# Kernel optimization log

Hardware: AMD Instinct MI355X
Metric: run time of the kernel (lower is better)

Reference implementation:

```python
import jax, jax.numpy as jnp
import numpy as np

K = 8
NUM_BLOCKS = 4
ALPHA = K / (K + 1)  # 8/9


def _knn_norm_adj(xyz, k):
    """xyz: (B, 3, N) -> symmetric-normalized GCN adjacency (B, N, N).

    Mirrors knn_point(k, xyz, xyz) -> indices[:, 1:] -> get_adjacency_matrix,
    then the (input-independent) DenseGCNConv normalization: self loops set to 1,
    deg clamped >= 1, D^-1/2 A D^-1/2. adj is identical for every GCN call, so
    it is normalized once here.
    """
    x2 = jnp.sum(xyz * xyz, axis=1)                       # (B, N)
    inner = jnp.einsum('bci,bcj->bij', xyz, xyz)          # (B, N, N)
    dist = x2[:, :, None] + x2[:, None, :] - 2.0 * inner  # squared pairwise dist
    _, idx = jax.lax.top_k(-dist, k)                      # (B, N, k); self (dist 0) first
    nbr = idx[:, :, 1:]                                   # drop self -> k-1 neighbors
    B, N = x2.shape
    adj = jnp.zeros((B, N, N), xyz.dtype)
    adj = adj.at[jnp.arange(B)[:, None, None],
                 jnp.arange(N)[None, :, None], nbr].set(1.0)
    ar = jnp.arange(N)
    adj = adj.at[:, ar, ar].set(1.0)                      # add_loop=True
    dis = jnp.clip(jnp.sum(adj, axis=-1), 1.0, None) ** -0.5  # (B, N)
    return dis[:, :, None] * adj * dis[:, None, :]


def setup_inputs() -> dict:
    key = jax.random.key(0)
    ks = jax.random.split(key, 6)
    B, N, C = 16, 2048, 128
    s = 1.0 / np.sqrt(C).astype(np.float32)
    return {
        'xyz': jax.random.normal(ks[0], (B, 3, N), jnp.float32),
        'points': jax.random.normal(ks[1], (B, C, N), jnp.float32),
        'Wc': jax.random.normal(ks[2], (4, C, C), jnp.float32) * s,   # nn.Linear weights (out,in)
        'Wg': jax.random.normal(ks[3], (4, C, C), jnp.float32) * s,   # DenseGCNConv lin weights
        'Wuc': jax.random.normal(ks[4], (6, C), jnp.float32) * s,
        'Wug': jax.random.normal(ks[5], (6, C), jnp.float32) * s,
    }


def reference(xyz, points, Wc, Wg, Wuc, Wug):
    adj = _knn_norm_adj(xyz, K)                 # (B, N, N)
    pts = jnp.swapaxes(points, 1, 2)            # (B, N, C) channel-last internally
    for i in range(NUM_BLOCKS):
        shortcut = pts
        act = jax.nn.relu(pts)
        center = jnp.einsum('bnc,dc->bnd', act, Wc[i])                 # Linear on relu(points)
        grouped = adj @ jnp.einsum('bnc,dc->bnd', shortcut, Wg[i])     # DenseGCNConv on shortcut
        pts = (1.0 - ALPHA) * grouped + ALPHA * center + shortcut
    # unpool head
    points_xyz = jnp.einsum('bnd,od->bno', pts, Wuc)                   # (B, N, 6)
    grouped_xyz = adj @ jnp.einsum('bnd,od->bno', pts, Wug)            # (B, N, 6)
    new = ALPHA * points_xyz + (1.0 - ALPHA) * grouped_xyz
    B, N, _ = new.shape
    new = jnp.swapaxes(new, 1, 2).reshape(B, 3, 2, N) + xyz[:, :, None, :]
    new_xyz = new.reshape(B, 3, 2 * N)
    return new_xyz, jnp.swapaxes(pts, 1, 2)     # ((B,3,2N), (B,C,N))
```

## Files before the change

### kernel.cpp

```cpp
#include <hip/hip_runtime.h>
#include <hip/hip_bf16.h>

static constexpr int NB = 16;
static constexpr int NP = 2048;
static constexpr int NC = 128;
#define ALPHA_F ((float)(8.0/9.0))
#define OMA_F   ((float)(1.0 - 8.0/9.0))

typedef __attribute__((ext_vector_type(8))) short bfrag;
typedef __attribute__((ext_vector_type(4))) float ffrag;

union BU { bfrag v; uint4 u; unsigned int w[4]; };

__device__ inline void split2(float x, float y, unsigned& hi, unsigned& lo) {
    __hip_bfloat162 h = __float22bfloat162_rn(make_float2(x, y));
    float2 hb = __bfloat1622float2(h);
    __hip_bfloat162 l = __float22bfloat162_rn(make_float2(x - hb.x, y - hb.y));
    __builtin_memcpy(&hi, &h, 4);
    __builtin_memcpy(&lo, &l, 4);
}

__device__ inline void split1(float x, unsigned short& h, unsigned short& l) {
    __hip_bfloat16 hb = __float2bfloat16(x);
    float hf = __bfloat162float(hb);
    __hip_bfloat16 lb = __float2bfloat16(x - hf);
    __builtin_memcpy(&h, &hb, 2);
    __builtin_memcpy(&l, &lb, 2);
}

__global__ __launch_bounds__(256) void knn_kernel(const float* __restrict__ xyz,
                                                  int* __restrict__ nbr) {
    __shared__ float4 sp[NP];
    __shared__ float  md[64][33];
    __shared__ int    mi[64][33];
    int b = blockIdx.y;
    const float* X = xyz + (size_t)b * 3 * NP;
    for (int m = threadIdx.x; m < NP; m += 256) {
        float x = X[m], y = X[NP + m], z = X[2 * NP + m];
        sp[m] = make_float4(x, y, z, x * x + y * y + z * z);
    }
    __syncthreads();

    int tid = threadIdx.x;
    int p = tid >> 2;
    int q = tid & 3;
    int base = blockIdx.x * 64;
    int n = base + p;
    float4 me = sp[n];
    float xi = me.x, yi = me.y, zi = me.z, qi = me.w;

    float gd[8]; int gi[8];
#pragma unroll
    for (int t = 0; t < 8; ++t) { gd[t] = 3.4e38f; gi[t] = 0; }
#pragma unroll 1
    for (int g = 0; g < 64; ++g) {
        float gm = 3.4e38f;
#pragma unroll
        for (int i = 0; i < 8; ++i) {
            int j = (g * 8 + i) * 4 + q;
            float4 c4v = sp[j];
            float inner = xi * c4v.x + yi * c4v.y + zi * c4v.z;
            float d = qi + c4v.w - 2.0f * inner;
            gm = fminf(gm, d);
        }
        bool c[8];
#pragma unroll
        for (int t = 0; t < 8; ++t) c[t] = gm < gd[t];
#pragma unroll
        for (int t = 7; t >= 1; --t) {
            gd[t] = c[t - 1] ? gd[t - 1] : (c[t] ? gm : gd[t]);
            gi[t] = c[t - 1] ? gi[t - 1] : (c[t] ? g : gi[t]);
        }
        gd[0] = c[0] ? gm : gd[0];
        gi[0] = c[0] ? g : gi[0];
    }

    unsigned long long mask = 0ull;
#pragma unroll
    for (int t = 0; t < 8; ++t) mask |= (1ull << gi[t]);

    float bd[8]; int bi[8];
#pragma unroll
    for (int t = 0; t < 8; ++t) { bd[t] = 3.4e38f; bi[t] = 0; }
    while (mask) {
        int g = (int)__builtin_ctzll(mask);
        mask &= (mask - 1ull);
#pragma unroll
        for (int i = 0; i < 8; ++i) {
            int j = (g * 8 + i) * 4 + q;
            float4 c4v = sp[j];
            float inner = xi * c4v.x + yi * c4v.y + zi * c4v.z;
            float d = qi + c4v.w - 2.0f * inner;
            bool c[8];
#pragma unroll
            for (int t = 0; t < 8; ++t) c[t] = d < bd[t];
#pragma unroll
            for (int t = 7; t >= 1; --t) {
                bd[t] = c[t - 1] ? bd[t - 1] : (c[t] ? d : bd[t]);
                bi[t] = c[t - 1] ? bi[t - 1] : (c[t] ? j : bi[t]);
            }
            bd[0] = c[0] ? d : bd[0];
            bi[0] = c[0] ? j : bi[0];
        }
    }
#pragma unroll
    for (int t = 0; t < 8; ++t) {
        md[p][q * 8 + t] = bd[t];
        mi[p][q * 8 + t] = bi[t];
    }
    __syncthreads();

    if (tid < 64) {
        float fd[8]; int fi[8];
#pragma unroll
        for (int t = 0; t < 8; ++t) { fd[t] = 3.4e38f; fi[t] = 0; }
#pragma unroll 4
        for (int cc = 0; cc < 32; ++cc) {
            float d = md[tid][cc];
            int j = mi[tid][cc];
            bool c[8];
#pragma unroll
            for (int t = 0; t < 8; ++t) c[t] = d < fd[t];
#pragma unroll
            for (int t = 7; t >= 1; --t) {
                fd[t] = c[t - 1] ? fd[t - 1] : (c[t] ? d : fd[t]);
                fi[t] = c[t - 1] ? fi[t - 1] : (c[t] ? j : fi[t]);
            }
            fd[0] = c[0] ? d : fd[0];
            fi[0] = c[0] ? j : fi[0];
        }
        int row = b * NP + base + tid;
#pragma unroll
        for (int t = 0; t < 7; ++t) nbr[row * 7 + t] = fi[t + 1];
    }
}

__global__ __launch_bounds__(256) void transpose_kernel(const float* __restrict__ in,
                                                        float* __restrict__ out,
                                                        int R, int S) {
    __shared__ float t[32][33];
    int b = blockIdx.z;
    int s0 = blockIdx.x * 32, r0 = blockIdx.y * 32;
    const float* I = in + (size_t)b * R * S;
    float* O = out + (size_t)b * R * S;
#pragma unroll
    for (int i = 0; i < 4; ++i) {
        int r = r0 + threadIdx.y + i * 8;
        t[threadIdx.y + i * 8][threadIdx.x] = I[(size_t)r * S + s0 + threadIdx.x];
    }
    __syncthreads();
#pragma unroll
    for (int i = 0; i < 4; ++i) {
        int s = s0 + threadIdx.y + i * 8;
        O[(size_t)s * R + r0 + threadIdx.x] = t[threadIdx.x][threadIdx.y + i * 8];
    }
}

__global__ __launch_bounds__(256) void prep_w_kernel(const float* __restrict__ Wc,
                                                     const float* __restrict__ Wg,
                                                     uint4* __restrict__ WP) {
    int t = blockIdx.x * 256 + threadIdx.x;
    int ncol = t & 127;
    int quad = (t >> 7) & 3;
    int s = (t >> 9) & 3;
    int mat = (t >> 11) & 1;
    int layer = t >> 12;
    const float* W = (mat ? Wg : Wc) + (size_t)layer * NC * NC + (size_t)ncol * NC + s * 32 + quad * 8;
    float4 a = *((const float4*)W);
    float4 b = *((const float4*)(W + 4));
    BU hi, lo;
    split2(a.x, a.y, hi.w[0], lo.w[0]);
    split2(a.z, a.w, hi.w[1], lo.w[1]);
    split2(b.x, b.y, hi.w[2], lo.w[2]);
    split2(b.z, b.w, hi.w[3], lo.w[3]);
    WP[t * 2] = hi.u;
    WP[t * 2 + 1] = lo.u;
}

template <int MODE>
__global__ __launch_bounds__(512) void gemm_fused_kernel(const float* __restrict__ Asrc,
                                                         const float* __restrict__ Y2in,
                                                         const int* __restrict__ nbr,
                                                         const uint4* __restrict__ WPc,
                                                         const uint4* __restrict__ WPg,
                                                         float* __restrict__ Zout,
                                                         float* __restrict__ Y2out) {
    __shared__ unsigned short AhT[64][136];
    __shared__ unsigned short AlT[64][136];
    __shared__ int s_nb[448];
    int tid = threadIdx.x;
    int wid = tid >> 6, lane = tid & 63;
    int quad = lane >> 4, l15 = lane & 15;
    int xcd = blockIdx.x & 7;
    int slot = blockIdx.x >> 3;
    int bb = xcd * 2 + (slot >> 5);
    int n0 = (slot & 31) << 6;
    size_t m0 = (size_t)bb * NP + n0;
    int ncol = wid * 16 + l15;

    BU Bch[4], Bcl[4], Bgh[4], Bgl[4];
#pragma unroll
    for (int s = 0; s < 4; ++s) {
        int idx = ((s * 4 + quad) * 128 + ncol) * 2;
        Bch[s].u = WPc[idx];
        Bcl[s].u = WPc[idx + 1];
        Bgh[s].u = WPg[idx];
        Bgl[s].u = WPg[idx + 1];
    }

    if (MODE == 1) {
        if (tid < 448) s_nb[tid] = nbr[m0 * 7 + tid];
        __syncthreads();
        size_t bbase = (size_t)bb * NP;
#pragma unroll 1
        for (int it = 0; it < 4; ++it) {
            int f = tid + it * 512;
            int r = f >> 5, c4 = (f & 31) * 4;
            size_t row = m0 + r;
            float4 z = *((const float4*)(Asrc + row * NC + c4));
            float4 acc = *((const float4*)(Y2in + row * NC + c4));
#pragma unroll
            for (int t = 0; t < 7; ++t) {
                int j = s_nb[r * 7 + t];
                float4 v = *((const float4*)(Y2in + (bbase + (size_t)j) * NC + c4));
                acc.x += v.x; acc.y += v.y; acc.z += v.z; acc.w += v.w;
            }
            float4 a;
            a.x = OMA_F * (0.125f * acc.x) + z.x;
            a.y = OMA_F * (0.125f * acc.y) + z.y;
            a.z = OMA_F * (0.125f * acc.z) + z.z;
            a.w = OMA_F * (0.125f * acc.w) + z.w;
            unsigned h01, l01, h23, l23;
            split2(a.x, a.y, h01, l01);
            split2(a.z, a.w, h23, l23);
            *((uint2*)&AhT[r][c4]) = make_uint2(h01, h23);
            *((uint2*)&AlT[r][c4]) = make_uint2(l01, l23);
        }
    } else {
#pragma unroll
        for (int it = 0; it < 4; ++it) {
            int f = tid + it * 512;
            int c = f >> 4, rq = (f & 15) * 4;
            float4 v = *((const float4*)(Asrc + ((size_t)bb * NC + c) * NP + n0 + rq));
            float vv[4] = {v.x, v.y, v.z, v.w};
#pragma unroll
            for (int k = 0; k < 4; ++k) {
                unsigned short h, l;
                split1(vv[k], h, l);
                AhT[rq + k][c] = h;
                AlT[rq + k][c] = l;
            }
        }
    }
    __syncthreads();

    ffrag accC[4], accG[4];
#pragma unroll
    for (int mt = 0; mt < 4; ++mt) { accC[mt] = (ffrag)0.0f; accG[mt] = (ffrag)0.0f; }

#pragma unroll
    for (int s = 0; s < 4; ++s) {
#pragma unroll
        for (int mt = 0; mt < 4; ++mt) {
            int m = mt * 16 + l15;
            int k = s * 32 + quad * 8;
            BU ah, al, rh, rl;
            ah.u = *((const uint4*)&AhT[m][k]);
            al.u = *((const uint4*)&AlT[m][k]);
#pragma unroll
            for (int w = 0; w < 4; ++w) {
                unsigned msk = ((ah.w[w] & 0x80008000u) >> 15) * 0xFFFFu;
                rh.w[w] = ah.w[w] & ~msk;
                rl.w[w] = al.w[w] & ~msk;
            }
            accC[mt] = __builtin_amdgcn_mfma_f32_16x16x32_bf16(rh.v, Bch[s].v, accC[mt], 0, 0, 0);
            accC[mt] = __builtin_amdgcn_mfma_f32_16x16x32_bf16(rh.v, Bcl[s].v, accC[mt], 0, 0, 0);
            accC[mt] = __builtin_amdgcn_mfma_f32_16x16x32_bf16(rl.v, Bch[s].v, accC[mt], 0, 0, 0);
            accG[mt] = __builtin_amdgcn_mfma_f32_16x16x32_bf16(ah.v, Bgh[s].v, accG[mt], 0, 0, 0);
            accG[mt] = __builtin_amdgcn_mfma_f32_16x16x32_bf16(ah.v, Bgl[s].v, accG[mt], 0, 0, 0);
            accG[mt] = __builtin_amdgcn_mfma_f32_16x16x32_bf16(al.v, Bgh[s].v, accG[mt], 0, 0, 0);
        }
    }

#pragma unroll
    for (int mt = 0; mt < 4; ++mt) {
        int rbase = mt * 16 + quad * 4;
#pragma unroll
        for (int r = 0; r < 4; ++r) {
            int rr = rbase + r;
            unsigned hb = ((unsigned)AhT[rr][ncol]) << 16;
            unsigned lb = ((unsigned)AlT[rr][ncol]) << 16;
            float hp, lp;
            __builtin_memcpy(&hp, &hb, 4);
            __builtin_memcpy(&lp, &lb, 4);
            float p = hp + lp;
            size_t idx = (m0 + rr) * NC + ncol;
            Zout[idx] = p + ALPHA_F * accC[mt][r];
            Y2out[idx] = accG[mt][r];
        }
    }
}

__global__ __launch_bounds__(256) void agg_kernel(const float* __restrict__ Z,
                                                  const float* __restrict__ Y2,
                                                  const int* __restrict__ nbr,
                                                  float* __restrict__ Pout) {
    int tid = threadIdx.x;
    int lane = tid & 31, rl = tid >> 5;
    int xcd = blockIdx.x & 7;
    int slot = blockIdx.x >> 3;
    int bb = xcd * 2 + (slot >> 8);
    int rblk = slot & 255;
    size_t row = ((size_t)bb << 11) + rblk * 8 + rl;
    const int* nb = nbr + row * 7;
    size_t off = row * NC + lane * 4;
    float4 ys = *((const float4*)(Y2 + off));
    size_t bbase = (size_t)bb * NP * NC;
#pragma unroll
    for (int t = 0; t < 7; ++t) {
        int j = nb[t];
        float4 v = *((const float4*)(Y2 + bbase + (size_t)j * NC + lane * 4));
        ys.x += v.x; ys.y += v.y; ys.z += v.z; ys.w += v.w;
    }
    float4 z = *((const float4*)(Z + off));
    float4 o;
    o.x = OMA_F * (0.125f * ys.x) + z.x;
    o.y = OMA_F * (0.125f * ys.y) + z.y;
    o.z = OMA_F * (0.125f * ys.z) + z.z;
    o.w = OMA_F * (0.125f * ys.w) + z.w;
    *((float4*)(Pout + off)) = o;
}

__global__ __launch_bounds__(256) void final_gemm_kernel(const float* __restrict__ P,
                                                         const float* __restrict__ Wuc,
                                                         const float* __restrict__ Wug,
                                                         float* __restrict__ U) {
    __shared__ float s1[6 * NC], s2[6 * NC];
    for (int m = threadIdx.x; m < 6 * NC; m += 256) { s1[m] = Wuc[m]; s2[m] = Wug[m]; }
    __syncthreads();
    size_t row = (size_t)blockIdx.x * 256 + threadIdx.x;
    const float4* prow = (const float4*)(P + row * NC);
    float a1[6] = {0, 0, 0, 0, 0, 0}, a2[6] = {0, 0, 0, 0, 0, 0};
#pragma unroll 4
    for (int c4 = 0; c4 < NC / 4; ++c4) {
        float4 p = prow[c4];
#pragma unroll
        for (int o = 0; o < 6; ++o) {
            float4 w1 = *((const float4*)&s1[o * NC + c4 * 4]);
            float4 w2 = *((const float4*)&s2[o * NC + c4 * 4]);
            a1[o] += p.x * w1.x + p.y * w1.y + p.z * w1.z + p.w * w1.w;
            a2[o] += p.x * w2.x + p.y * w2.y + p.z * w2.z + p.w * w2.w;
        }
    }
#pragma unroll
    for (int o = 0; o < 6; ++o) {
        U[row * 12 + o] = a1[o];
        U[row * 12 + 6 + o] = a2[o];
    }
}

__global__ __launch_bounds__(256) void final_out_kernel(const float* __restrict__ U,
                                                        const int* __restrict__ nbr,
                                                        const float* __restrict__ xyz,
                                                        float* __restrict__ out) {
    size_t row = (size_t)blockIdx.x * 256 + threadIdx.x;
    int b = (int)(row >> 11), n = (int)(row & 2047);
    const int* nb = nbr + row * 7;
    float u1[6], u2[6];
#pragma unroll
    for (int o = 0; o < 6; ++o) { u1[o] = U[row * 12 + o]; u2[o] = U[row * 12 + 6 + o]; }
#pragma unroll
    for (int t = 0; t < 7; ++t) {
        int j = nb[t];
        const float* Uj = U + ((size_t)b * NP + j) * 12 + 6;
#pragma unroll
        for (int o = 0; o < 6; ++o) u2[o] += Uj[o];
    }
#pragma unroll
    for (int c = 0; c < 3; ++c)
#pragma unroll
        for (int s = 0; s < 2; ++s) {
            int o = c * 2 + s;
            float val = ALPHA_F * u1[o] + OMA_F * (0.125f * u2[o])
                      + xyz[(size_t)b * 3 * NP + (size_t)c * NP + n];
            out[(size_t)b * 3 * 2 * NP + (size_t)c * 2 * NP + (size_t)s * NP + n] = val;
        }
}

extern "C" void kernel_launch(void* const* d_in, const int* in_sizes, int n_in,
                              void* d_out, int out_size, void* d_ws, size_t ws_size,
                              hipStream_t stream) {
    const float* xyz    = (const float*)d_in[0];
    const float* points = (const float*)d_in[1];
    const float* Wc     = (const float*)d_in[2];
    const float* Wg     = (const float*)d_in[3];
    const float* Wuc    = (const float*)d_in[4];
    const float* Wug    = (const float*)d_in[5];
    float* out = (float*)d_out;

    char* ws = (char*)d_ws;
    size_t o = 0;
    int* nbr  = (int*)(ws + o);     o += (size_t)NB * NP * 7 * 4;
    uint4* WP = (uint4*)(ws + o);   o += (size_t)32768 * 16;
    float* Za = (float*)(ws + o);   o += (size_t)NB * NP * NC * 4;
    float* Ya = (float*)(ws + o);   o += (size_t)NB * NP * NC * 4;
    float* Zb = (float*)(ws + o);   o += (size_t)NB * NP * NC * 4;
    float* Yb = (float*)(ws + o);   o += (size_t)NB * NP * NC * 4;
    float* U  = (float*)(ws + o);   o += (size_t)NB * NP * 12 * 4;

    const int GEMM_GRID = NB * NP / 64;
    #define WPC(L) (WP + (size_t)((L) * 2 + 0) * 4096)
    #define WPG(L) (WP + (size_t)((L) * 2 + 1) * 4096)

    prep_w_kernel<<<64, 256, 0, stream>>>(Wc, Wg, WP);
    knn_kernel<<<dim3(NP / 64, NB), 256, 0, stream>>>(xyz, nbr);
    gemm_fused_kernel<0><<<GEMM_GRID, 512, 0, stream>>>(points, nullptr, nullptr,
        WPC(0), WPG(0), Za, Ya);
    gemm_fused_kernel<1><<<GEMM_GRID, 512, 0, stream>>>(Za, Ya, nbr,
        WPC(1), WPG(1), Zb, Yb);
    gemm_fused_kernel<1><<<GEMM_GRID, 512, 0, stream>>>(Zb, Yb, nbr,
        WPC(2), WPG(2), Za, Ya);
    gemm_fused_kernel<1><<<GEMM_GRID, 512, 0, stream>>>(Za, Ya, nbr,
        WPC(3), WPG(3), Zb, Yb);
    float* P5 = Za;
    agg_kernel<<<dim3(NB * NP / 8), 256, 0, stream>>>(Zb, Yb, nbr, P5);
    final_gemm_kernel<<<dim3(NB * NP / 256), 256, 0, stream>>>(P5, Wuc, Wug, U);
    final_out_kernel<<<dim3(NB * NP / 256), 256, 0, stream>>>(U, nbr, xyz, out);
    transpose_kernel<<<dim3(NC / 32, NP / 32, NB), dim3(32, 8), 0, stream>>>(
        P5, out + (size_t)NB * 3 * 2 * NP, NP, NC);
}
```

Baseline: 225.6 us.

## Precompute packed xyz candidates globally and read them via wave-uniform scalar loads in kNN

A merged prep kernel now builds packed (x,y,z,|p|^2) candidate records in global memory alongside the weight split, replacing the separate weight-prep kernel. The kNN kernel drops its per-block shared-memory staging of all 2048 points and instead gives each wave a contiguous 512-candidate slice, with one lane per query point and wave-uniform candidate addresses so loads can become scalar/broadcast. This removes the redundant per-block staging, the barrier and LDS traffic, and one kernel launch. In exchange it adds a global buffer, and the refine pass uses per-lane divergent global loads.

```diff
diff --git a/kernel.cpp b/kernel.cpp
--- a/kernel.cpp
+++ b/kernel.cpp
@@ -28,25 +28,51 @@
     __builtin_memcpy(&l, &lb, 2);
 }
 
-__global__ __launch_bounds__(256) void knn_kernel(const float* __restrict__ xyz,
+__global__ __launch_bounds__(256) void prep_kernel(const float* __restrict__ Wc,
+                                                   const float* __restrict__ Wg,
+                                                   const float* __restrict__ xyz,
+                                                   uint4* __restrict__ WP,
+                                                   float4* __restrict__ cand) {
+    if (blockIdx.x < 64) {
+        int t = blockIdx.x * 256 + threadIdx.x;
+        int ncol = t & 127;
+        int quad = (t >> 7) & 3;
+        int s = (t >> 9) & 3;
+        int mat = (t >> 11) & 1;
+        int layer = t >> 12;
+        const float* W = (mat ? Wg : Wc) + (size_t)layer * NC * NC + (size_t)ncol * NC + s * 32 + quad * 8;
+        float4 a = *((const float4*)W);
+        float4 b = *((const float4*)(W + 4));
+        BU hi, lo;
+        split2(a.x, a.y, hi.w[0], lo.w[0]);
+        split2(a.z, a.w, hi.w[1], lo.w[1]);
+        split2(b.x, b.y, hi.w[2], lo.w[2]);
+        split2(b.z, b.w, hi.w[3], lo.w[3]);
+        WP[t * 2] = hi.u;
+        WP[t * 2 + 1] = lo.u;
+    } else {
+        int idx = (blockIdx.x - 64) * 256 + threadIdx.x;
+        int b = idx >> 11, m = idx & 2047;
+        const float* X = xyz + (size_t)b * 3 * NP;
+        float x = X[m], y = X[NP + m], z = X[2 * NP + m];
+        cand[idx] = make_float4(x, y, z, x * x + y * y + z * z);
+    }
+}
+
+__global__ __launch_bounds__(256) void knn_kernel(const float4* __restrict__ cand,
                                                   int* __restrict__ nbr) {
-    __shared__ float4 sp[NP];
-    __shared__ float  md[64][33];
-    __shared__ int    mi[64][33];
+    __shared__ float md[64][33];
+    __shared__ int   mi[64][33];
+    int tid = threadIdx.x;
+    int lane = tid & 63;
+    int w = __builtin_amdgcn_readfirstlane(tid >> 6);
     int b = blockIdx.y;
-    const float* X = xyz + (size_t)b * 3 * NP;
-    for (int m = threadIdx.x; m < NP; m += 256) {
-        float x = X[m], y = X[NP + m], z = X[2 * NP + m];
-        sp[m] = make_float4(x, y, z, x * x + y * y + z * z);
-    }
-    __syncthreads();
-
-    int tid = threadIdx.x;
-    int p = tid >> 2;
-    int q = tid & 3;
     int base = blockIdx.x * 64;
-    int n = base + p;
-    float4 me = sp[n];
+    const float4* C = cand + ((size_t)b << 11);
+    const float4* CS = C + (w << 9);
+
+    int n = base + lane;
+    float4 me = C[n];
     float xi = me.x, yi = me.y, zi = me.z, qi = me.w;
 
     float gd[8]; int gi[8];
@@ -54,13 +80,14 @@
     for (int t = 0; t < 8; ++t) { gd[t] = 3.4e38f; gi[t] = 0; }
 #pragma unroll 1
     for (int g = 0; g < 64; ++g) {
+        float4 cv[8];
+#pragma unroll
+        for (int i = 0; i < 8; ++i) cv[i] = CS[g * 8 + i];
         float gm = 3.4e38f;
 #pragma unroll
         for (int i = 0; i < 8; ++i) {
-            int j = (g * 8 + i) * 4 + q;
-            float4 c4v = sp[j];
-            float inner = xi * c4v.x + yi * c4v.y + zi * c4v.z;
-            float d = qi + c4v.w - 2.0f * inner;
+            float inner = xi * cv[i].x + yi * cv[i].y + zi * cv[i].z;
+            float d = qi + cv[i].w - 2.0f * inner;
             gm = fminf(gm, d);
         }
         bool c[8];
@@ -85,10 +112,11 @@
     while (mask) {
         int g = (int)__builtin_ctzll(mask);
         mask &= (mask - 1ull);
+        int jb = (w << 9) + g * 8;
 #pragma unroll
         for (int i = 0; i < 8; ++i) {
-            int j = (g * 8 + i) * 4 + q;
-            float4 c4v = sp[j];
+            int j = jb + i;
+            float4 c4v = C[j];
             float inner = xi * c4v.x + yi * c4v.y + zi * c4v.z;
             float d = qi + c4v.w - 2.0f * inner;
             bool c[8];
@@ -105,8 +133,8 @@
     }
 #pragma unroll
     for (int t = 0; t < 8; ++t) {
-        md[p][q * 8 + t] = bd[t];
-        mi[p][q * 8 + t] = bi[t];
+        md[lane][w * 8 + t] = bd[t];
+        mi[lane][w * 8 + t] = bi[t];
     }
     __syncthreads();
 
@@ -154,27 +182,6 @@
         int s = s0 + threadIdx.y + i * 8;
         O[(size_t)s * R + r0 + threadIdx.x] = t[threadIdx.x][threadIdx.y + i * 8];
     }
-}
-
-__global__ __launch_bounds__(256) void prep_w_kernel(const float* __restrict__ Wc,
-                                                     const float* __restrict__ Wg,
-                                                     uint4* __restrict__ WP) {
-    int t = blockIdx.x * 256 + threadIdx.x;
-    int ncol = t & 127;
-    int quad = (t >> 7) & 3;
-    int s = (t >> 9) & 3;
-    int mat = (t >> 11) & 1;
-    int layer = t >> 12;
-    const float* W = (mat ? Wg : Wc) + (size_t)layer * NC * NC + (size_t)ncol * NC + s * 32 + quad * 8;
-    float4 a = *((const float4*)W);
-    float4 b = *((const float4*)(W + 4));
-    BU hi, lo;
-    split2(a.x, a.y, hi.w[0], lo.w[0]);
-    split2(a.z, a.w, hi.w[1], lo.w[1]);
-    split2(b.x, b.y, hi.w[2], lo.w[2]);
-    split2(b.z, b.w, hi.w[3], lo.w[3]);
-    WP[t * 2] = hi.u;
-    WP[t * 2 + 1] = lo.u;
 }
 
 template <int MODE>
@@ -400,20 +407,21 @@
 
     char* ws = (char*)d_ws;
     size_t o = 0;
-    int* nbr  = (int*)(ws + o);     o += (size_t)NB * NP * 7 * 4;
-    uint4* WP = (uint4*)(ws + o);   o += (size_t)32768 * 16;
-    float* Za = (float*)(ws + o);   o += (size_t)NB * NP * NC * 4;
-    float* Ya = (float*)(ws + o);   o += (size_t)NB * NP * NC * 4;
-    float* Zb = (float*)(ws + o);   o += (size_t)NB * NP * NC * 4;
-    float* Yb = (float*)(ws + o);   o += (size_t)NB * NP * NC * 4;
-    float* U  = (float*)(ws + o);   o += (size_t)NB * NP * 12 * 4;
+    int* nbr    = (int*)(ws + o);    o += (size_t)NB * NP * 7 * 4;
+    uint4* WP   = (uint4*)(ws + o);  o += (size_t)32768 * 16;
+    float4* CAND = (float4*)(ws + o); o += (size_t)NB * NP * 16;
+    float* Za = (float*)(ws + o);    o += (size_t)NB * NP * NC * 4;
+    float* Ya = (float*)(ws + o);    o += (size_t)NB * NP * NC * 4;
+    float* Zb = (float*)(ws + o);    o += (size_t)NB * NP * NC * 4;
+    float* Yb = (float*)(ws + o);    o += (size_t)NB * NP * NC * 4;
+    float* U  = (float*)(ws + o);    o += (size_t)NB * NP * 12 * 4;
 
     const int GEMM_GRID = NB * NP / 64;
     #define WPC(L) (WP + (size_t)((L) * 2 + 0) * 4096)
     #define WPG(L) (WP + (size_t)((L) * 2 + 1) * 4096)
 
-    prep_w_kernel<<<64, 256, 0, stream>>>(Wc, Wg, WP);
-    knn_kernel<<<dim3(NP / 64, NB), 256, 0, stream>>>(xyz, nbr);
+    prep_kernel<<<192, 256, 0, stream>>>(Wc, Wg, xyz, WP, CAND);
+    knn_kernel<<<dim3(NP / 64, NB), 256, 0, stream>>>(CAND, nbr);
     gemm_fused_kernel<0><<<GEMM_GRID, 512, 0, stream>>>(points, nullptr, nullptr,
         WPC(0), WPG(0), Za, Ya);
     gemm_fused_kernel<1><<<GEMM_GRID, 512, 0, stream>>>(Za, Ya, nbr,
```

Result: slower. 237.9 us (+5.4%).
